# Optimization experiments

Measured on AMD Instinct MI355X. Metric: run time of the kernel, lower is better.

The kernel has to match this reference:

```python
import jax, jax.numpy as jnp
import numpy as np
from jax import lax

DIM = 256
B = 2
EPS = 1e-5


def setup_inputs() -> dict:
    key = jax.random.key(0)
    ks = jax.random.split(key, 8)
    d = DIM
    s = 0.02
    return {
        "x": jax.random.normal(ks[0], (B, d, d, d), jnp.float32),
        "conv_w": jax.random.normal(ks[1], (d, 1, 7, 7), jnp.float32) * s,
        "conv_b": jax.random.normal(ks[2], (d,), jnp.float32) * s,
        "ln_g": jnp.ones((d,), jnp.float32),
        "ln_b": jnp.zeros((d,), jnp.float32),
        "w1": jax.random.normal(ks[3], (4 * d, d), jnp.float32) * s,
        "b1": jax.random.normal(ks[4], (4 * d,), jnp.float32) * s,
        "w2": jax.random.normal(ks[5], (d, 4 * d), jnp.float32) * s,
        "b2": jax.random.normal(ks[6], (d,), jnp.float32) * s,
    }


def reference(x, conv_w, conv_b, ln_g, ln_b, w1, b1, w2, b2):
    dim = x.shape[1]
    # depthwise 7x7 conv, padding=3, NCHW / OIHW (O=dim, I=1)
    y = lax.conv_general_dilated(
        x, conv_w, window_strides=(1, 1), padding=((3, 3), (3, 3)),
        feature_group_count=dim, dimension_numbers=("NCHW", "OIHW", "NCHW"))
    y = y + conv_b[None, :, None, None]
    # LayerNorm over LAST axis (W) -- faithful to the original (un-permuted) code
    mu = jnp.mean(y, axis=-1, keepdims=True)
    var = jnp.mean(jnp.square(y - mu), axis=-1, keepdims=True)
    y = (y - mu) * lax.rsqrt(var + EPS) * ln_g + ln_b
    # MLP over last axis: dim -> 4*dim -> dim, exact GELU (torch default)
    y = jax.nn.gelu(jnp.einsum("bchw,ow->bcho", y, w1) + b1, approximate=False)
    y = jnp.einsum("bcho,wo->bchw", y, w2) + b2
    # rearrange 'b h w c -> b c h w' == transpose (0,3,1,2), then residual
    return x + jnp.transpose(y, (0, 3, 1, 2))
```

## Files before the change

### kernel.cpp

```cpp
#include <hip/hip_runtime.h>
#include <hip/hip_bf16.h>
#include <math.h>

using short8 = __attribute__((ext_vector_type(8))) short;
using f32x4  = __attribute__((ext_vector_type(4))) float;

static __device__ __forceinline__ f32x4 mfma16(short8 a, short8 b, f32x4 c){
    return __builtin_amdgcn_mfma_f32_16x16x32_bf16(a, b, c, 0, 0, 0);
}

static __device__ __forceinline__ unsigned short bf16of(float f){
    unsigned int u = __float_as_uint(f);
    unsigned int lsb = (u >> 16) & 1u;
    u += 0x7fffu + lsb;
    return (unsigned short)(u >> 16);
}

static __device__ __forceinline__ unsigned int pk2(float lo, float hi){
    return __builtin_amdgcn_perm(__float_as_uint(hi) + 0x8000u,
                                 __float_as_uint(lo) + 0x8000u, 0x07060302u);
}

static __device__ __forceinline__ float gelu_fast(float x){
    float e = __builtin_amdgcn_exp2f(-2.4554669596f * x);
    return x * __builtin_amdgcn_rcpf(1.0f + e);
}

__global__ __launch_bounds__(256) void prep_weights(
    const float* __restrict__ w1, const float* __restrict__ w2,
    unsigned short* __restrict__ w1p, unsigned short* __restrict__ w2p)
{
    int t = blockIdx.x * 256 + threadIdx.x;
    int lane = t & 63;
    if (t < 32768){
        int g = t;
        int ks  = (g >> 6) & 7;
        int n16 = g >> 9;
        int o = n16*16 + (lane & 15);
        int k = ks*32 + (lane >> 4)*8;
        const float* src = w1 + o*256 + k;
        unsigned short* dst = w1p + (size_t)g*8;
        #pragma unroll
        for (int j = 0; j < 8; ++j) dst[j] = bf16of(src[j]);
    } else {
        int g = t - 32768;
        int ksg = (g >> 6) & 31;
        int n16 = g >> 11;
        int n = n16*16 + (lane & 15);
        int k = ksg*32 + (lane >> 4)*8;
        const float* src = w2 + n*1024 + k;
        unsigned short* dst = w2p + (size_t)g*8;
        #pragma unroll
        for (int j = 0; j < 8; ++j) dst[j] = bf16of(src[j]);
    }
}

#define CH 16
#define XR (CH + 6)
#define XWV 66
#define XW 264

__global__ __launch_bounds__(256) void conv_ln_kernel(
    const float* __restrict__ x, const float* __restrict__ conv_w,
    const float* __restrict__ conv_b, const float* __restrict__ ln_g,
    const float* __restrict__ ln_b, unsigned short* __restrict__ ynormF)
{
    __shared__ float xt[XR * XW];
    __shared__ unsigned short ytn[CH * 264];

    const int tid = threadIdx.x;
    const int blk = blockIdx.x;
    const int ht = blk & 15;
    const int c  = (blk >> 4) & 255;
    const int b  = blk >> 12;
    const int h0 = ht * CH;

    const float* xplane = x + (((size_t)(b*256 + c)) << 16);

    for (int i = tid; i < XR*XWV; i += 256){
        int ir = i / XWV;
        int cc = i - ir*XWV;
        int gh = h0 - 3 + ir;
        float4 v = make_float4(0.f, 0.f, 0.f, 0.f);
        if ((unsigned)gh < 256u && (unsigned)(cc - 1) < 64u)
            v = *reinterpret_cast<const float4*>(xplane + gh*256 + (cc - 1)*4);
        *reinterpret_cast<float4*>(&xt[ir*XW + cc*4]) = v;
    }

    float cwr[49];
    #pragma unroll
    for (int i = 0; i < 49; ++i) cwr[i] = conv_w[c*49 + i];
    const float cb = conv_b[c];

    __syncthreads();

    const int wq = tid & 63;
    const int hs = tid >> 6;
    float acc[4][4] = {};

    #pragma unroll
    for (int d = 0; d < 10; ++d){
        int ir = hs*4 + d;
        float4 ra = *reinterpret_cast<const float4*>(&xt[ir*XW + wq*4]);
        float4 rb = *reinterpret_cast<const float4*>(&xt[ir*XW + wq*4 + 4]);
        float4 rc = *reinterpret_cast<const float4*>(&xt[ir*XW + wq*4 + 8]);
        float rr[12] = {ra.x, ra.y, ra.z, ra.w, rb.x, rb.y, rb.z, rb.w,
                        rc.x, rc.y, rc.z, rc.w};
        #pragma unroll
        for (int ro = 0; ro < 4; ++ro){
            int dh = d - ro;
            if (dh >= 0 && dh <= 6){
                #pragma unroll
                for (int dw = 0; dw < 7; ++dw){
                    float wv = cwr[dh*7 + dw];
                    #pragma unroll
                    for (int cc = 0; cc < 4; ++cc)
                        acc[ro][cc] = fmaf(rr[cc + dw + 1], wv, acc[ro][cc]);
                }
            }
        }
    }

    #pragma unroll
    for (int ro = 0; ro < 4; ++ro)
        #pragma unroll
        for (int cc = 0; cc < 4; ++cc)
            acc[ro][cc] += cb;

    const float4 lgv = *reinterpret_cast<const float4*>(ln_g + wq*4);
    const float4 lbv = *reinterpret_cast<const float4*>(ln_b + wq*4);
    const float lg[4] = {lgv.x, lgv.y, lgv.z, lgv.w};
    const float lb[4] = {lbv.x, lbv.y, lbv.z, lbv.w};

    #pragma unroll
    for (int ro = 0; ro < 4; ++ro){
        float s  = acc[ro][0] + acc[ro][1] + acc[ro][2] + acc[ro][3];
        float ss = acc[ro][0]*acc[ro][0] + acc[ro][1]*acc[ro][1]
                 + acc[ro][2]*acc[ro][2] + acc[ro][3]*acc[ro][3];
        #pragma unroll
        for (int off = 32; off > 0; off >>= 1){
            s  += __shfl_xor(s, off);
            ss += __shfl_xor(ss, off);
        }
        float mu  = s * (1.f/256.f);
        float var = ss * (1.f/256.f) - mu*mu;
        float rs  = rsqrtf(var + 1e-5f);
        unsigned int u01, u23;
        {
            float o0 = (acc[ro][0] - mu)*rs*lg[0] + lb[0];
            float o1 = (acc[ro][1] - mu)*rs*lg[1] + lb[1];
            float o2 = (acc[ro][2] - mu)*rs*lg[2] + lb[2];
            float o3 = (acc[ro][3] - mu)*rs*lg[3] + lb[3];
            u01 = (unsigned int)bf16of(o0) | ((unsigned int)bf16of(o1) << 16);
            u23 = (unsigned int)bf16of(o2) | ((unsigned int)bf16of(o3) << 16);
        }
        uint2 pv; pv.x = u01; pv.y = u23;
        *reinterpret_cast<uint2*>(&ytn[(hs*4 + ro)*264 + wq*4]) = pv;
    }

    __syncthreads();

    {
        const int l   = tid & 63;
        const int wv  = tid >> 6;
        const int l15w = l & 15, kgw = l >> 4;
        const int tile = (((b*256 + c)*256 + h0) >> 6);
        const int mf = (h0 >> 4) & 3;
        uint4* dst = reinterpret_cast<uint4*>(ynormF) + (size_t)tile*2048;
        #pragma unroll
        for (int it = 0; it < 2; ++it){
            int ks = wv*2 + it;
            uint4 v = *reinterpret_cast<const uint4*>(ytn + l15w*264 + ks*32 + kgw*8);
            dst[(ks*4 + mf)*64 + l] = v;
        }
    }
}

__global__ __launch_bounds__(256, 2) void mlp_kernel(
    const unsigned short* __restrict__ ynormF,
    const short* __restrict__ w1p, const short* __restrict__ w2p,
    const float* __restrict__ b1, const float* __restrict__ b2,
    const float* __restrict__ x, float* __restrict__ out)
{
    __shared__ __align__(16) char smem[65536];
    short* Ash = (short*)smem;
    short* Hs0 = (short*)(smem + 32768);
    short* Hs1 = (short*)(smem + 49152);

    const int tid  = threadIdx.x;
    const int lane = tid & 63;
    const int wid  = tid >> 6;
    const int tile = blockIdx.x;
    const int M0 = tile * 64;
    const int b = M0 >> 16, c = (M0 >> 8) & 255, h0 = M0 & 255;

    const int l15  = lane & 15;
    const int kg   = lane >> 4;

    {
        const uint4* src = reinterpret_cast<const uint4*>(ynormF) + (size_t)tile*2048;
        uint4* dst = reinterpret_cast<uint4*>(Ash);
        for (int i = tid; i < 2048; i += 256) dst[i] = src[i];
    }
    __syncthreads();

    f32x4 acc2[4][4];
    #pragma unroll
    for (int nfi = 0; nfi < 4; ++nfi){
        float4 bv = *reinterpret_cast<const float4*>(b2 + (wid*4 + nfi)*16 + kg*4);
        f32x4 b4 = {bv.x, bv.y, bv.z, bv.w};
        #pragma unroll
        for (int mf = 0; mf < 4; ++mf) acc2[mf][nfi] = b4;
    }

    f32x4 accA[4][2], accB[4][2];
    short8 pw2[4];

    auto gemm1 = [&](int oc, f32x4 (&acc1)[4][2]){
        #pragma unroll
        for (int nfi = 0; nfi < 2; ++nfi){
            float4 bv = *reinterpret_cast<const float4*>(
                b1 + oc*128 + (wid*2 + nfi)*16 + kg*4);
            f32x4 bi = {bv.x, bv.y, bv.z, bv.w};
            #pragma unroll
            for (int mf = 0; mf < 4; ++mf) acc1[mf][nfi] = bi;
        }
        #pragma unroll
        for (int ks = 0; ks < 8; ++ks){
            short8 afr[4], bfr[2];
            #pragma unroll
            for (int mf = 0; mf < 4; ++mf)
                afr[mf] = *reinterpret_cast<const short8*>(
                    Ash + ((ks*4 + mf)*64 + lane)*8);
            #pragma unroll
            for (int nfi = 0; nfi < 2; ++nfi)
                bfr[nfi] = *reinterpret_cast<const short8*>(
                    w1p + ((size_t)(((oc*8 + wid*2 + nfi)*8 + ks)*64 + lane)) * 8);
            #pragma unroll
            for (int mf = 0; mf < 4; ++mf)
                #pragma unroll
                for (int nfi = 0; nfi < 2; ++nfi)
                    acc1[mf][nfi] = mfma16(bfr[nfi], afr[mf], acc1[mf][nfi]);
        }
    };

    auto gelu_store = [&](f32x4 (&acc1)[4][2], short* Hb){
        #pragma unroll
        for (int nfi = 0; nfi < 2; ++nfi){
            int chunkbase = (wid*2 + nfi)*2 + (kg >> 1);
            int osub = (kg & 1) << 2;
            #pragma unroll
            for (int mf = 0; mf < 4; ++mf){
                int m = mf*16 + l15;
                uint2 pv;
                pv.x = pk2(gelu_fast(acc1[mf][nfi][0]), gelu_fast(acc1[mf][nfi][1]));
                pv.y = pk2(gelu_fast(acc1[mf][nfi][2]), gelu_fast(acc1[mf][nfi][3]));
                *reinterpret_cast<uint2*>(
                    Hb + m*128 + ((chunkbase ^ (m & 7)) << 3) + osub) = pv;
            }
        }
    };

    auto prefetch_pw2 = [&](int oc){
        #pragma unroll
        for (int nfi = 0; nfi < 4; ++nfi)
            pw2[nfi] = *reinterpret_cast<const short8*>(
                w2p + ((size_t)(((wid*4 + nfi)*32 + oc*4 + 0)*64 + lane)) * 8);
    };

    auto gemm2f = [&](int oc, short* Hb){
        #pragma unroll
        for (int ks = 0; ks < 4; ++ks){
            short8 hfr[4], wfr[4];
            #pragma unroll
            for (int mf = 0; mf < 4; ++mf){
                int row = mf*16 + l15;
                hfr[mf] = *reinterpret_cast<const short8*>(
                    Hb + row*128 + (((ks*4 + kg) ^ (l15 & 7)) << 3));
            }
            if (ks == 0){
                #pragma unroll
                for (int nfi = 0; nfi < 4; ++nfi) wfr[nfi] = pw2[nfi];
            } else {
                #pragma unroll
                for (int nfi = 0; nfi < 4; ++nfi)
                    wfr[nfi] = *reinterpret_cast<const short8*>(
                        w2p + ((size_t)(((wid*4 + nfi)*32 + oc*4 + ks)*64 + lane)) * 8);
            }
            #pragma unroll
            for (int mf = 0; mf < 4; ++mf)
                #pragma unroll
                for (int nfi = 0; nfi < 4; ++nfi)
                    acc2[mf][nfi] = mfma16(wfr[nfi], hfr[mf], acc2[mf][nfi]);
        }
    };

    gemm1(0, accA);
    gelu_store(accA, Hs0);
    gemm1(1, accB);
    prefetch_pw2(0);
    __syncthreads();

    #pragma unroll
    for (int oc = 0; oc < 8; ++oc){
        short* Hcur = (oc & 1) ? Hs1 : Hs0;
        gemm2f(oc, Hcur);
        if (oc < 7){
            f32x4 (&accR)[4][2] = ((oc + 1) & 1) ? accB : accA;
            gelu_store(accR, (oc & 1) ? Hs0 : Hs1);
        }
        if (oc < 6){
            f32x4 (&accW)[4][2] = ((oc + 2) & 1) ? accB : accA;
            gemm1(oc + 2, accW);
        }
        if (oc < 7){
            prefetch_pw2(oc + 1);
            __syncthreads();
        }
    }

    #pragma unroll
    for (int nfi = 0; nfi < 4; ++nfi){
        #pragma unroll
        for (int r = 0; r < 4; ++r){
            int w = (wid*4 + nfi)*16 + kg*4 + r;
            size_t base = ((size_t)b << 24) + ((size_t)w << 16) + (c << 8) + h0 + l15;
            #pragma unroll
            for (int mf = 0; mf < 4; ++mf){
                size_t o = base + mf*16;
                out[o] = acc2[mf][nfi][r] + x[o];
            }
        }
    }
}

extern "C" void kernel_launch(void* const* d_in, const int* in_sizes, int n_in,
                              void* d_out, int out_size, void* d_ws, size_t ws_size,
                              hipStream_t stream)
{
    const float* x      = (const float*)d_in[0];
    const float* conv_w = (const float*)d_in[1];
    const float* conv_b = (const float*)d_in[2];
    const float* ln_g   = (const float*)d_in[3];
    const float* ln_b   = (const float*)d_in[4];
    const float* w1     = (const float*)d_in[5];
    const float* b1     = (const float*)d_in[6];
    const float* w2     = (const float*)d_in[7];
    const float* b2     = (const float*)d_in[8];
    float* out = (float*)d_out;

    unsigned short* ynormF = (unsigned short*)d_ws;
    unsigned short* w1p    = (unsigned short*)((char*)d_ws + 67108864);
    unsigned short* w2p    = (unsigned short*)((char*)d_ws + 67108864 + 524288);

    hipLaunchKernelGGL(prep_weights, dim3(256), dim3(256), 0, stream, w1, w2, w1p, w2p);
    hipLaunchKernelGGL(conv_ln_kernel, dim3(8192), dim3(256), 0, stream,
                       x, conv_w, conv_b, ln_g, ln_b, ynormF);
    hipLaunchKernelGGL(mlp_kernel, dim3(2048), dim3(256), 0, stream,
                       ynormF, (const short*)w1p, (const short*)w2p, b1, b2, x, out);
}
```

Before: 235.2 us.

## Fuse depthwise conv and LayerNorm into the MLP kernel, dropping the intermediate buffer

Merges the conv+LayerNorm kernel into the MLP kernel. Each 64-row tile now computes its own conv and LayerNorm in four 16-row sub-steps, staging them in shared memory that is later reused for the hidden activations. This removes the 64 MB bf16 intermediate write and read and one kernel launch. The trade-offs are that the conv phase now runs at the MLP kernel's lower occupancy of 2 blocks per CU, and it adds per-sub-step barriers with no overlap between the conv and GEMM phases.

```diff
diff --git a/kernel.cpp b/kernel.cpp
--- a/kernel.cpp
+++ b/kernel.cpp
@@ -55,135 +55,22 @@
     }
 }
 
-#define CH 16
-#define XR (CH + 6)
+#define XR 22
 #define XWV 66
 #define XW 264
 
-__global__ __launch_bounds__(256) void conv_ln_kernel(
+__global__ __launch_bounds__(256, 2) void fused_kernel(
     const float* __restrict__ x, const float* __restrict__ conv_w,
     const float* __restrict__ conv_b, const float* __restrict__ ln_g,
-    const float* __restrict__ ln_b, unsigned short* __restrict__ ynormF)
-{
-    __shared__ float xt[XR * XW];
-    __shared__ unsigned short ytn[CH * 264];
-
-    const int tid = threadIdx.x;
-    const int blk = blockIdx.x;
-    const int ht = blk & 15;
-    const int c  = (blk >> 4) & 255;
-    const int b  = blk >> 12;
-    const int h0 = ht * CH;
-
-    const float* xplane = x + (((size_t)(b*256 + c)) << 16);
-
-    for (int i = tid; i < XR*XWV; i += 256){
-        int ir = i / XWV;
-        int cc = i - ir*XWV;
-        int gh = h0 - 3 + ir;
-        float4 v = make_float4(0.f, 0.f, 0.f, 0.f);
-        if ((unsigned)gh < 256u && (unsigned)(cc - 1) < 64u)
-            v = *reinterpret_cast<const float4*>(xplane + gh*256 + (cc - 1)*4);
-        *reinterpret_cast<float4*>(&xt[ir*XW + cc*4]) = v;
-    }
-
-    float cwr[49];
-    #pragma unroll
-    for (int i = 0; i < 49; ++i) cwr[i] = conv_w[c*49 + i];
-    const float cb = conv_b[c];
-
-    __syncthreads();
-
-    const int wq = tid & 63;
-    const int hs = tid >> 6;
-    float acc[4][4] = {};
-
-    #pragma unroll
-    for (int d = 0; d < 10; ++d){
-        int ir = hs*4 + d;
-        float4 ra = *reinterpret_cast<const float4*>(&xt[ir*XW + wq*4]);
-        float4 rb = *reinterpret_cast<const float4*>(&xt[ir*XW + wq*4 + 4]);
-        float4 rc = *reinterpret_cast<const float4*>(&xt[ir*XW + wq*4 + 8]);
-        float rr[12] = {ra.x, ra.y, ra.z, ra.w, rb.x, rb.y, rb.z, rb.w,
-                        rc.x, rc.y, rc.z, rc.w};
-        #pragma unroll
-        for (int ro = 0; ro < 4; ++ro){
-            int dh = d - ro;
-            if (dh >= 0 && dh <= 6){
-                #pragma unroll
-                for (int dw = 0; dw < 7; ++dw){
-                    float wv = cwr[dh*7 + dw];
-                    #pragma unroll
-                    for (int cc = 0; cc < 4; ++cc)
-                        acc[ro][cc] = fmaf(rr[cc + dw + 1], wv, acc[ro][cc]);
-                }
-            }
-        }
-    }
-
-    #pragma unroll
-    for (int ro = 0; ro < 4; ++ro)
-        #pragma unroll
-        for (int cc = 0; cc < 4; ++cc)
-            acc[ro][cc] += cb;
-
-    const float4 lgv = *reinterpret_cast<const float4*>(ln_g + wq*4);
-    const float4 lbv = *reinterpret_cast<const float4*>(ln_b + wq*4);
-    const float lg[4] = {lgv.x, lgv.y, lgv.z, lgv.w};
-    const float lb[4] = {lbv.x, lbv.y, lbv.z, lbv.w};
-
-    #pragma unroll
-    for (int ro = 0; ro < 4; ++ro){
-        float s  = acc[ro][0] + acc[ro][1] + acc[ro][2] + acc[ro][3];
-        float ss = acc[ro][0]*acc[ro][0] + acc[ro][1]*acc[ro][1]
-                 + acc[ro][2]*acc[ro][2] + acc[ro][3]*acc[ro][3];
-        #pragma unroll
-        for (int off = 32; off > 0; off >>= 1){
-            s  += __shfl_xor(s, off);
-            ss += __shfl_xor(ss, off);
-        }
-        float mu  = s * (1.f/256.f);
-        float var = ss * (1.f/256.f) - mu*mu;
-        float rs  = rsqrtf(var + 1e-5f);
-        unsigned int u01, u23;
-        {
-            float o0 = (acc[ro][0] - mu)*rs*lg[0] + lb[0];
-            float o1 = (acc[ro][1] - mu)*rs*lg[1] + lb[1];
-            float o2 = (acc[ro][2] - mu)*rs*lg[2] + lb[2];
-            float o3 = (acc[ro][3] - mu)*rs*lg[3] + lb[3];
-            u01 = (unsigned int)bf16of(o0) | ((unsigned int)bf16of(o1) << 16);
-            u23 = (unsigned int)bf16of(o2) | ((unsigned int)bf16of(o3) << 16);
-        }
-        uint2 pv; pv.x = u01; pv.y = u23;
-        *reinterpret_cast<uint2*>(&ytn[(hs*4 + ro)*264 + wq*4]) = pv;
-    }
-
-    __syncthreads();
-
-    {
-        const int l   = tid & 63;
-        const int wv  = tid >> 6;
-        const int l15w = l & 15, kgw = l >> 4;
-        const int tile = (((b*256 + c)*256 + h0) >> 6);
-        const int mf = (h0 >> 4) & 3;
-        uint4* dst = reinterpret_cast<uint4*>(ynormF) + (size_t)tile*2048;
-        #pragma unroll
-        for (int it = 0; it < 2; ++it){
-            int ks = wv*2 + it;
-            uint4 v = *reinterpret_cast<const uint4*>(ytn + l15w*264 + ks*32 + kgw*8);
-            dst[(ks*4 + mf)*64 + l] = v;
-        }
-    }
-}
-
-__global__ __launch_bounds__(256, 2) void mlp_kernel(
-    const unsigned short* __restrict__ ynormF,
+    const float* __restrict__ ln_b,
     const short* __restrict__ w1p, const short* __restrict__ w2p,
     const float* __restrict__ b1, const float* __restrict__ b2,
-    const float* __restrict__ x, float* __restrict__ out)
+    float* __restrict__ out)
 {
     __shared__ __align__(16) char smem[65536];
     short* Ash = (short*)smem;
+    float* xt  = (float*)(smem + 32768);
+    unsigned short* ytn = (unsigned short*)(smem + 32768 + 23232);
     short* Hs0 = (short*)(smem + 32768);
     short* Hs1 = (short*)(smem + 49152);
 
@@ -198,9 +85,97 @@
     const int kg   = lane >> 4;
 
     {
-        const uint4* src = reinterpret_cast<const uint4*>(ynormF) + (size_t)tile*2048;
-        uint4* dst = reinterpret_cast<uint4*>(Ash);
-        for (int i = tid; i < 2048; i += 256) dst[i] = src[i];
+        const float* xplane = x + (((size_t)(b*256 + c)) << 16);
+
+        float cwr[49];
+        #pragma unroll
+        for (int i = 0; i < 49; ++i) cwr[i] = conv_w[c*49 + i];
+        const float cb = conv_b[c];
+
+        const int wq = tid & 63;
+        const int hs = tid >> 6;
+        const float4 lgv = *reinterpret_cast<const float4*>(ln_g + wq*4);
+        const float4 lbv = *reinterpret_cast<const float4*>(ln_b + wq*4);
+        const float lg[4] = {lgv.x, lgv.y, lgv.z, lgv.w};
+        const float lb[4] = {lbv.x, lbv.y, lbv.z, lbv.w};
+
+        for (int sub = 0; sub < 4; ++sub){
+            const int hb = h0 + sub*16;
+
+            for (int i = tid; i < XR*XWV; i += 256){
+                int ir = i / XWV;
+                int cc = i - ir*XWV;
+                int gh = hb - 3 + ir;
+                float4 v = make_float4(0.f, 0.f, 0.f, 0.f);
+                if ((unsigned)gh < 256u && (unsigned)(cc - 1) < 64u)
+                    v = *reinterpret_cast<const float4*>(xplane + gh*256 + (cc - 1)*4);
+                *reinterpret_cast<float4*>(&xt[ir*XW + cc*4]) = v;
+            }
+            __syncthreads();
+
+            float acc[4][4] = {};
+            #pragma unroll
+            for (int d = 0; d < 10; ++d){
+                int ir = hs*4 + d;
+                float4 ra = *reinterpret_cast<const float4*>(&xt[ir*XW + wq*4]);
+                float4 rb = *reinterpret_cast<const float4*>(&xt[ir*XW + wq*4 + 4]);
+                float4 rc = *reinterpret_cast<const float4*>(&xt[ir*XW + wq*4 + 8]);
+                float rr[12] = {ra.x, ra.y, ra.z, ra.w, rb.x, rb.y, rb.z, rb.w,
+                                rc.x, rc.y, rc.z, rc.w};
+                #pragma unroll
+                for (int ro = 0; ro < 4; ++ro){
+                    int dh = d - ro;
+                    if (dh >= 0 && dh <= 6){
+                        #pragma unroll
+                        for (int dw = 0; dw < 7; ++dw){
+                            float wv = cwr[dh*7 + dw];
+                            #pragma unroll
+                            for (int cc = 0; cc < 4; ++cc)
+                                acc[ro][cc] = fmaf(rr[cc + dw + 1], wv, acc[ro][cc]);
+                        }
+                    }
+                }
+            }
+            #pragma unroll
+            for (int ro = 0; ro < 4; ++ro)
+                #pragma unroll
+                for (int cc = 0; cc < 4; ++cc)
+                    acc[ro][cc] += cb;
+
+            #pragma unroll
+            for (int ro = 0; ro < 4; ++ro){
+                float s  = acc[ro][0] + acc[ro][1] + acc[ro][2] + acc[ro][3];
+                float ss = acc[ro][0]*acc[ro][0] + acc[ro][1]*acc[ro][1]
+                         + acc[ro][2]*acc[ro][2] + acc[ro][3]*acc[ro][3];
+                #pragma unroll
+                for (int off = 32; off > 0; off >>= 1){
+                    s  += __shfl_xor(s, off);
+                    ss += __shfl_xor(ss, off);
+                }
+                float mu  = s * (1.f/256.f);
+                float var = ss * (1.f/256.f) - mu*mu;
+                float rs  = rsqrtf(var + 1e-5f);
+                float o0 = (acc[ro][0] - mu)*rs*lg[0] + lb[0];
+                float o1 = (acc[ro][1] - mu)*rs*lg[1] + lb[1];
+                float o2 = (acc[ro][2] - mu)*rs*lg[2] + lb[2];
+                float o3 = (acc[ro][3] - mu)*rs*lg[3] + lb[3];
+                uint2 pv;
+                pv.x = (unsigned int)bf16of(o0) | ((unsigned int)bf16of(o1) << 16);
+                pv.y = (unsigned int)bf16of(o2) | ((unsigned int)bf16of(o3) << 16);
+                *reinterpret_cast<uint2*>(&ytn[(hs*4 + ro)*264 + wq*4]) = pv;
+            }
+            __syncthreads();
+
+            {
+                uint4* dstu = reinterpret_cast<uint4*>(Ash);
+                #pragma unroll
+                for (int it = 0; it < 2; ++it){
+                    int ks = wid*2 + it;
+                    uint4 v = *reinterpret_cast<const uint4*>(ytn + l15*264 + ks*32 + kg*8);
+                    dstu[(ks*4 + sub)*64 + lane] = v;
+                }
+            }
+        }
     }
     __syncthreads();
 
@@ -349,13 +324,11 @@
     const float* b2     = (const float*)d_in[8];
     float* out = (float*)d_out;
 
-    unsigned short* ynormF = (unsigned short*)d_ws;
-    unsigned short* w1p    = (unsigned short*)((char*)d_ws + 67108864);
-    unsigned short* w2p    = (unsigned short*)((char*)d_ws + 67108864 + 524288);
+    unsigned short* w1p = (unsigned short*)d_ws;
+    unsigned short* w2p = (unsigned short*)((char*)d_ws + 524288);
 
     hipLaunchKernelGGL(prep_weights, dim3(256), dim3(256), 0, stream, w1, w2, w1p, w2p);
-    hipLaunchKernelGGL(conv_ln_kernel, dim3(8192), dim3(256), 0, stream,
-                       x, conv_w, conv_b, ln_g, ln_b, ynormF);
-    hipLaunchKernelGGL(mlp_kernel, dim3(2048), dim3(256), 0, stream,
-                       ynormF, (const short*)w1p, (const short*)w2p, b1, b2, x, out);
-}
+    hipLaunchKernelGGL(fused_kernel, dim3(2048), dim3(256), 0, stream,
+                       x, conv_w, conv_b, ln_g, ln_b,
+                       (const short*)w1p, (const short*)w2p, b1, b2, out);
+}
```

After: 240.5 us. 1.02x slower.

## Fold weight prep into conv+LN kernel and use 512-thread blocks

Applied to the files above, without the earlier changes.

Merges the separate bf16 weight-packing kernel into the conv/LayerNorm kernel as 128 extra blocks, removing one kernel launch. The conv block grows to 512 threads, so each thread computes 2 output rows instead of 4, which adds parallelism but increases redundant shared-memory row reads (8 rows loaded per 2 outputs versus 10 per 4). Register pressure per thread drops, while the 49 conv weights are still held per thread.

```diff
diff --git a/kernel.cpp b/kernel.cpp
--- a/kernel.cpp
+++ b/kernel.cpp
@@ -26,50 +26,51 @@
     return x * __builtin_amdgcn_rcpf(1.0f + e);
 }
 
-__global__ __launch_bounds__(256) void prep_weights(
-    const float* __restrict__ w1, const float* __restrict__ w2,
-    unsigned short* __restrict__ w1p, unsigned short* __restrict__ w2p)
-{
-    int t = blockIdx.x * 256 + threadIdx.x;
-    int lane = t & 63;
-    if (t < 32768){
-        int g = t;
-        int ks  = (g >> 6) & 7;
-        int n16 = g >> 9;
-        int o = n16*16 + (lane & 15);
-        int k = ks*32 + (lane >> 4)*8;
-        const float* src = w1 + o*256 + k;
-        unsigned short* dst = w1p + (size_t)g*8;
-        #pragma unroll
-        for (int j = 0; j < 8; ++j) dst[j] = bf16of(src[j]);
-    } else {
-        int g = t - 32768;
-        int ksg = (g >> 6) & 31;
-        int n16 = g >> 11;
-        int n = n16*16 + (lane & 15);
-        int k = ksg*32 + (lane >> 4)*8;
-        const float* src = w2 + n*1024 + k;
-        unsigned short* dst = w2p + (size_t)g*8;
-        #pragma unroll
-        for (int j = 0; j < 8; ++j) dst[j] = bf16of(src[j]);
-    }
-}
-
 #define CH 16
 #define XR (CH + 6)
 #define XWV 66
 #define XW 264
 
-__global__ __launch_bounds__(256) void conv_ln_kernel(
+__global__ __launch_bounds__(512) void conv_ln_prep_kernel(
     const float* __restrict__ x, const float* __restrict__ conv_w,
     const float* __restrict__ conv_b, const float* __restrict__ ln_g,
-    const float* __restrict__ ln_b, unsigned short* __restrict__ ynormF)
+    const float* __restrict__ ln_b, unsigned short* __restrict__ ynormF,
+    const float* __restrict__ w1, const float* __restrict__ w2,
+    unsigned short* __restrict__ w1p, unsigned short* __restrict__ w2p)
 {
     __shared__ float xt[XR * XW];
     __shared__ unsigned short ytn[CH * 264];
 
     const int tid = threadIdx.x;
     const int blk = blockIdx.x;
+
+    if (blk >= 8192){
+        int t = (blk - 8192)*512 + tid;
+        int lane = t & 63;
+        if (t < 32768){
+            int g = t;
+            int ks  = (g >> 6) & 7;
+            int n16 = g >> 9;
+            int o = n16*16 + (lane & 15);
+            int k = ks*32 + (lane >> 4)*8;
+            const float* src = w1 + o*256 + k;
+            unsigned short* dst = w1p + (size_t)g*8;
+            #pragma unroll
+            for (int j = 0; j < 8; ++j) dst[j] = bf16of(src[j]);
+        } else {
+            int g = t - 32768;
+            int ksg = (g >> 6) & 31;
+            int n16 = g >> 11;
+            int n = n16*16 + (lane & 15);
+            int k = ksg*32 + (lane >> 4)*8;
+            const float* src = w2 + n*1024 + k;
+            unsigned short* dst = w2p + (size_t)g*8;
+            #pragma unroll
+            for (int j = 0; j < 8; ++j) dst[j] = bf16of(src[j]);
+        }
+        return;
+    }
+
     const int ht = blk & 15;
     const int c  = (blk >> 4) & 255;
     const int b  = blk >> 12;
@@ -77,7 +78,7 @@
 
     const float* xplane = x + (((size_t)(b*256 + c)) << 16);
 
-    for (int i = tid; i < XR*XWV; i += 256){
+    for (int i = tid; i < XR*XWV; i += 512){
         int ir = i / XWV;
         int cc = i - ir*XWV;
         int gh = h0 - 3 + ir;
@@ -96,18 +97,18 @@
 
     const int wq = tid & 63;
     const int hs = tid >> 6;
-    float acc[4][4] = {};
-
-    #pragma unroll
-    for (int d = 0; d < 10; ++d){
-        int ir = hs*4 + d;
+    float acc[2][4] = {};
+
+    #pragma unroll
+    for (int d = 0; d < 8; ++d){
+        int ir = hs*2 + d;
         float4 ra = *reinterpret_cast<const float4*>(&xt[ir*XW + wq*4]);
         float4 rb = *reinterpret_cast<const float4*>(&xt[ir*XW + wq*4 + 4]);
         float4 rc = *reinterpret_cast<const float4*>(&xt[ir*XW + wq*4 + 8]);
         float rr[12] = {ra.x, ra.y, ra.z, ra.w, rb.x, rb.y, rb.z, rb.w,
                         rc.x, rc.y, rc.z, rc.w};
         #pragma unroll
-        for (int ro = 0; ro < 4; ++ro){
+        for (int ro = 0; ro < 2; ++ro){
             int dh = d - ro;
             if (dh >= 0 && dh <= 6){
                 #pragma unroll
@@ -122,7 +123,7 @@
     }
 
     #pragma unroll
-    for (int ro = 0; ro < 4; ++ro)
+    for (int ro = 0; ro < 2; ++ro)
         #pragma unroll
         for (int cc = 0; cc < 4; ++cc)
             acc[ro][cc] += cb;
@@ -133,7 +134,7 @@
     const float lb[4] = {lbv.x, lbv.y, lbv.z, lbv.w};
 
     #pragma unroll
-    for (int ro = 0; ro < 4; ++ro){
+    for (int ro = 0; ro < 2; ++ro){
         float s  = acc[ro][0] + acc[ro][1] + acc[ro][2] + acc[ro][3];
         float ss = acc[ro][0]*acc[ro][0] + acc[ro][1]*acc[ro][1]
                  + acc[ro][2]*acc[ro][2] + acc[ro][3]*acc[ro][3];
@@ -145,34 +146,27 @@
         float mu  = s * (1.f/256.f);
         float var = ss * (1.f/256.f) - mu*mu;
         float rs  = rsqrtf(var + 1e-5f);
-        unsigned int u01, u23;
-        {
-            float o0 = (acc[ro][0] - mu)*rs*lg[0] + lb[0];
-            float o1 = (acc[ro][1] - mu)*rs*lg[1] + lb[1];
-            float o2 = (acc[ro][2] - mu)*rs*lg[2] + lb[2];
-            float o3 = (acc[ro][3] - mu)*rs*lg[3] + lb[3];
-            u01 = (unsigned int)bf16of(o0) | ((unsigned int)bf16of(o1) << 16);
-            u23 = (unsigned int)bf16of(o2) | ((unsigned int)bf16of(o3) << 16);
-        }
-        uint2 pv; pv.x = u01; pv.y = u23;
-        *reinterpret_cast<uint2*>(&ytn[(hs*4 + ro)*264 + wq*4]) = pv;
+        float o0 = (acc[ro][0] - mu)*rs*lg[0] + lb[0];
+        float o1 = (acc[ro][1] - mu)*rs*lg[1] + lb[1];
+        float o2 = (acc[ro][2] - mu)*rs*lg[2] + lb[2];
+        float o3 = (acc[ro][3] - mu)*rs*lg[3] + lb[3];
+        uint2 pv;
+        pv.x = (unsigned int)bf16of(o0) | ((unsigned int)bf16of(o1) << 16);
+        pv.y = (unsigned int)bf16of(o2) | ((unsigned int)bf16of(o3) << 16);
+        *reinterpret_cast<uint2*>(&ytn[(hs*2 + ro)*264 + wq*4]) = pv;
     }
 
     __syncthreads();
 
     {
         const int l   = tid & 63;
-        const int wv  = tid >> 6;
+        const int ks  = tid >> 6;
         const int l15w = l & 15, kgw = l >> 4;
         const int tile = (((b*256 + c)*256 + h0) >> 6);
         const int mf = (h0 >> 4) & 3;
         uint4* dst = reinterpret_cast<uint4*>(ynormF) + (size_t)tile*2048;
-        #pragma unroll
-        for (int it = 0; it < 2; ++it){
-            int ks = wv*2 + it;
-            uint4 v = *reinterpret_cast<const uint4*>(ytn + l15w*264 + ks*32 + kgw*8);
-            dst[(ks*4 + mf)*64 + l] = v;
-        }
+        uint4 v = *reinterpret_cast<const uint4*>(ytn + l15w*264 + ks*32 + kgw*8);
+        dst[(ks*4 + mf)*64 + l] = v;
     }
 }
 
@@ -353,9 +347,8 @@
     unsigned short* w1p    = (unsigned short*)((char*)d_ws + 67108864);
     unsigned short* w2p    = (unsigned short*)((char*)d_ws + 67108864 + 524288);
 
-    hipLaunchKernelGGL(prep_weights, dim3(256), dim3(256), 0, stream, w1, w2, w1p, w2p);
-    hipLaunchKernelGGL(conv_ln_kernel, dim3(8192), dim3(256), 0, stream,
-                       x, conv_w, conv_b, ln_g, ln_b, ynormF);
+    hipLaunchKernelGGL(conv_ln_prep_kernel, dim3(8320), dim3(512), 0, stream,
+                       x, conv_w, conv_b, ln_g, ln_b, ynormF, w1, w2, w1p, w2p);
     hipLaunchKernelGGL(mlp_kernel, dim3(2048), dim3(256), 0, stream,
                        ynormF, (const short*)w1p, (const short*)w2p, b1, b2, x, out);
 }
```

Result: no change. 234.5 us (-0.3%).
